# Optimization experiments

Hardware: AMD Instinct MI355X
Metric: run time of the kernel (lower is better)

## Reference

```python
import jax, jax.numpy as jnp
import numpy as np

C = 512
C8 = C // 8
B, H, W = 4, 64, 64


def _conv1x1(x, w, b):
    # x: (B, Cin, H, W), w: (Cout, Cin), b: (Cout,)
    return jnp.einsum('oi,bihw->bohw', w, x) + b[None, :, None, None]


def setup_inputs() -> dict:
    key = jax.random.key(0)
    ks = jax.random.split(key, 16)
    s = 0.02
    inp = {
        'x': jax.random.normal(ks[0], (B, C, H, W), dtype=jnp.float32),
        'wpq': jax.random.normal(ks[1], (C8, C), dtype=jnp.float32) * s,
        'bpq': jnp.zeros((C8,), jnp.float32),
        'wpk': jax.random.normal(ks[2], (C8, C), dtype=jnp.float32) * s,
        'bpk': jnp.zeros((C8,), jnp.float32),
        'wpv': jax.random.normal(ks[3], (C, C), dtype=jnp.float32) * s,
        'bpv': jnp.zeros((C,), jnp.float32),
        'wcq': jax.random.normal(ks[4], (C, C), dtype=jnp.float32) * s,
        'bcq': jnp.zeros((C,), jnp.float32),
        'wck': jax.random.normal(ks[5], (C, C), dtype=jnp.float32) * s,
        'bck': jnp.zeros((C,), jnp.float32),
        'wcv': jax.random.normal(ks[6], (C, C), dtype=jnp.float32) * s,
        'bcv': jnp.zeros((C,), jnp.float32),
        # gammas are zero-init in torch; use small nonzero values so both
        # attention branches contribute to the output numerically.
        'gpos': jax.random.normal(ks[7], (1,), dtype=jnp.float32) * 0.1,
        'gchan': jax.random.normal(ks[8], (1,), dtype=jnp.float32) * 0.1,
    }
    return inp


def reference(x, wpq, bpq, wpk, bpk, wpv, bpv, wcq, bcq, wck, bck, wcv, bcv, gpos, gchan):
    b, c, h, w = x.shape
    n = h * w
    # ---- position attention ----
    pos_q = _conv1x1(x, wpq, bpq).reshape(b, C8, n)           # (b, C/8, N)
    pos_k = _conv1x1(x, wpk, bpk).reshape(b, C8, n)           # (b, C/8, N)
    pos_v = _conv1x1(x, wpv, bpv).reshape(b, c, n)            # (b, C, N)
    pos_attn = jax.nn.softmax(jnp.einsum('bcq,bck->bqk', pos_q, pos_k), axis=-1)  # (b, N, N)
    pos_out = jnp.einsum('bck,bqk->bcq', pos_v, pos_attn).reshape(b, c, h, w)
    pos_out = gpos * pos_out + x
    # ---- channel attention ----
    chan_q = _conv1x1(pos_out, wcq, bcq).reshape(b, c, n)
    chan_k = _conv1x1(pos_out, wck, bck).reshape(b, c, n)
    chan_v = _conv1x1(pos_out, wcv, bcv).reshape(b, c, n)
    chan_attn = jax.nn.softmax(jnp.einsum('bin,bjn->bij', chan_q, chan_k), axis=-1)  # (b, C, C)
    chan_out = jnp.einsum('bij,bjn->bin', chan_attn, chan_v).reshape(b, c, h, w)
    return gchan * chan_out + pos_out
```

## Files before the change

kernel.cpp:

```cpp
#include <hip/hip_runtime.h>
#include <hip/hip_bf16.h>
#include <math.h>

typedef __bf16 bf16;
typedef __attribute__((ext_vector_type(8))) __bf16 bf16x8;
typedef __attribute__((ext_vector_type(4))) __bf16 bf16x4;
typedef __attribute__((ext_vector_type(4))) float f32x4;

#define DEVI static __device__ __forceinline__

DEVI int swzb(int row, int ch) { return ((ch ^ (row & 7)) << 4); }

DEVI void gl_lds16(const void* g, void* l) {
  __builtin_amdgcn_global_load_lds(
      (const __attribute__((address_space(1))) unsigned int*)g,
      (__attribute__((address_space(3))) unsigned int*)l, 16, 0, 0);
}

template<int N> DEVI void wait_vm() {
  if constexpr (N == 0) asm volatile("s_waitcnt vmcnt(0)" ::: "memory");
  else if constexpr (N == 4) asm volatile("s_waitcnt vmcnt(4)" ::: "memory");
  else if constexpr (N == 6) asm volatile("s_waitcnt vmcnt(6)" ::: "memory");
  else if constexpr (N == 8) asm volatile("s_waitcnt vmcnt(8)" ::: "memory");
}
DEVI void sbar() {
  __builtin_amdgcn_sched_barrier(0);
  __builtin_amdgcn_s_barrier();
  __builtin_amdgcn_sched_barrier(0);
}

__global__ __launch_bounds__(256) void prep_weights(
    const float* __restrict__ wpq, const float* __restrict__ wpk,
    const float* __restrict__ wpv, const float* __restrict__ wcq,
    const float* __restrict__ wck, const float* __restrict__ wcv,
    const float* __restrict__ bpq, const float* __restrict__ bpk,
    bf16* __restrict__ wqk, bf16* __restrict__ wpvb, bf16* __restrict__ wcqb,
    bf16* __restrict__ wckb, bf16* __restrict__ wcvT, float* __restrict__ bqk)
{
  int i = blockIdx.x * 256 + threadIdx.x;
  switch (blockIdx.y) {
    case 0: if (i < 64*512)  wqk[i]          = (bf16)wpq[i]; break;
    case 1: if (i < 64*512)  wqk[64*512 + i] = (bf16)wpk[i]; break;
    case 2: if (i < 512*512) wpvb[i] = (bf16)wpv[i]; break;
    case 3: if (i < 512*512) wcqb[i] = (bf16)wcq[i]; break;
    case 4: if (i < 512*512) wckb[i] = (bf16)wck[i]; break;
    case 5: if (i < 512*512) { int t = i >> 9, j = i & 511; wcvT[i] = (bf16)wcv[j*512 + t]; } break;
    case 6: if (i < 64) bqk[i] = bpq[i]; else if (i < 128) bqk[i] = bpk[i - 64]; break;
  }
}

__global__ __launch_bounds__(256) void transpose_x(const float* __restrict__ x, bf16* __restrict__ xbT)
{
  __shared__ float t[32][33];
  int b = blockIdx.z, n0 = blockIdx.x * 32, c0 = blockIdx.y * 32;
  int tx = threadIdx.x & 31, ty = threadIdx.x >> 5;
#pragma unroll
  for (int i = 0; i < 4; ++i)
    t[ty + 8*i][tx] = x[((size_t)b*512 + c0 + ty + 8*i)*4096 + n0 + tx];
  __syncthreads();
#pragma unroll
  for (int i = 0; i < 4; ++i)
    xbT[((size_t)b*4096 + n0 + ty + 8*i)*512 + c0 + tx] = (bf16)t[tx][ty + 8*i];
}

struct GemmP {
  const bf16* A; const bf16* Bt; void* C;
  long aS, bS;
  long cSbytes;
  int lda, ldb, ldc, K;
  int remap;
  const float* biasM; const float* biasN;
  const float* e_bq; const float* e_v; const float* e_u; const float* e_bk; float e_nn;
  long vS, uS;
  const float* gchan; const float* Abv; const bf16* Pres; long abvS, presS;
};

template<int BM, int BN, int BIAS, int EPI>
__global__ __launch_bounds__(256) void gemm_k(GemmP p)
{
  constexpr int QF = BM / 32;
  constexpr int CF = BN / 32;
  constexpr int NBUF = (BM + BN <= 192) ? 3 : 2;
  constexpr int LOADS = (BM + BN) / 32;
  __shared__ __align__(16) char sa[NBUF][BM * 128];
  __shared__ __align__(16) char sb[NBUF][BN * 128];
  const int tid = threadIdx.x, lane = tid & 63, w = tid >> 6;
  const int g = lane >> 4, l15 = lane & 15;
  int bx = blockIdx.x, by = blockIdx.y, bz = blockIdx.z;
  if (p.remap) {
    int ph = blockIdx.x;
    bz = (ph & 7) >> 1;
    int idx = ((ph & 1) << 6) | (ph >> 3);
    bx = idx & 3; by = idx >> 2;
  }
  const int bm = bx * BM, bn = by * BN;
  const bf16* A  = p.A  + (size_t)bz * p.aS;
  const bf16* Bt = p.Bt + (size_t)bz * p.bS;
  char* Cb = (char*)p.C + (size_t)bz * p.cSbytes;
  const int wm = (w & 1) * (BM / 2), wn = (w >> 1) * (BN / 2);
  const int srow = tid >> 3, sch = tid & 7;

  f32x4 acc[QF][CF];
#pragma unroll
  for (int i = 0; i < QF; ++i)
#pragma unroll
    for (int j = 0; j < CF; ++j) acc[i][j] = f32x4{0.f, 0.f, 0.f, 0.f};

  auto stage = [&](int k0, int bi) {
#pragma unroll
    for (int it = 0; it < BM / 32; ++it) {
      int r = it * 32 + srow;
      gl_lds16(A + (size_t)(bm + r) * p.lda + k0 + ((sch ^ (r & 7)) * 8),
               sa[bi] + (it * 32 + w * 8) * 128);
    }
#pragma unroll
    for (int it = 0; it < BN / 32; ++it) {
      int r = it * 32 + srow;
      gl_lds16(Bt + (size_t)(bn + r) * p.ldb + k0 + ((sch ^ (r & 7)) * 8),
               sb[bi] + (it * 32 + w * 8) * 128);
    }
  };
  auto compute = [&](int bi) {
#pragma unroll
    for (int kc = 0; kc < 2; ++kc) {
      bf16x8 af[QF], bfr[CF];
#pragma unroll
      for (int qf = 0; qf < QF; ++qf) {
        int row = wm + 16 * qf + l15;
        af[qf] = *(const bf16x8*)(sa[bi] + row * 128 + swzb(row, g + 4 * kc));
      }
#pragma unroll
      for (int cf = 0; cf < CF; ++cf) {
        int row = wn + 16 * cf + l15;
        bfr[cf] = *(const bf16x8*)(sb[bi] + row * 128 + swzb(row, g + 4 * kc));
      }
      __builtin_amdgcn_s_setprio(1);
#pragma unroll
      for (int qf = 0; qf < QF; ++qf)
#pragma unroll
        for (int cf = 0; cf < CF; ++cf)
          acc[qf][cf] = __builtin_amdgcn_mfma_f32_16x16x32_bf16(af[qf], bfr[cf], acc[qf][cf], 0, 0, 0);
      __builtin_amdgcn_s_setprio(0);
    }
  };

  const int nk = p.K >> 6;
  if constexpr (NBUF == 3) {
    stage(0, 0);
    if (nk > 1) { stage(64, 1); wait_vm<LOADS>(); } else wait_vm<0>();
    sbar();
    int bi = 0;
    for (int t = 0; t < nk; ++t) {
      int b2 = bi + 2; if (b2 >= 3) b2 -= 3;
      if (t + 2 < nk) stage((t + 2) << 6, b2);
      compute(bi);
      if (t + 1 < nk) {
        if (t + 2 < nk) wait_vm<LOADS>(); else wait_vm<0>();
        sbar();
      }
      if (++bi == 3) bi = 0;
    }
  } else {
    stage(0, 0);
    __syncthreads();
    for (int t = 0; t < nk; ++t) {
      const int cur = t & 1;
      if (t + 1 < nk) stage((t + 1) << 6, cur ^ 1);
      compute(cur);
      __syncthreads();
    }
  }

  float gc = 0.f;
  const float* AbvB = nullptr; const bf16* PresB = nullptr;
  const float* eV = nullptr; const float* eU = nullptr;
  if (EPI == 3) { gc = p.gchan[0]; AbvB = p.Abv + (size_t)bz * p.abvS; PresB = p.Pres + (size_t)bz * p.presS; }
  if (EPI == 2) { eV = p.e_v + (size_t)bz * p.vS; eU = p.e_u + (size_t)bz * p.uS; }

#pragma unroll
  for (int qf = 0; qf < QF; ++qf)
#pragma unroll
    for (int cf = 0; cf < CF; ++cf)
#pragma unroll
      for (int r = 0; r < 4; ++r) {
        int m = bm + wm + 16 * qf + 4 * g + r;
        int n = bn + wn + 16 * cf + l15;
        float v = acc[qf][cf][r];
        if (BIAS == 1) v += p.biasM[m];
        if (BIAS == 2) v += p.biasN[n];
        size_t idx = (size_t)m * p.ldc + n;
        if (EPI == 0) ((bf16*)Cb)[idx] = (bf16)v;
        else if (EPI == 1) ((float*)Cb)[idx] = v;
        else if (EPI == 2) {
          v += p.e_bq[m] * eV[n] + eU[m] * p.e_bk[n] + p.e_nn * p.e_bq[m] * p.e_bk[n];
          ((float*)Cb)[idx] = v;
        } else {
          v = gc * (v + AbvB[m]) + (float)PresB[idx];
          ((float*)Cb)[idx] = v;
        }
      }
}

__global__ __launch_bounds__(512, 4) void flash_pos(
    const bf16* __restrict__ QKT, const bf16* __restrict__ Vv,
    const float* __restrict__ x, const float* __restrict__ gpos,
    bf16* __restrict__ Pb, bf16* __restrict__ PTb)
{
  extern __shared__ char sm[];
  char* Vlds = sm + 16384;
  char* Plds = sm + 49152;
  float* Och  = (float*)sm;
  float* lsum = (float*)(sm + 57344);

  const int tid = threadIdx.x, lane = tid & 63, w = tid >> 6;
  const int g = lane >> 4, l15 = lane & 15;
  const int wq = w & 3;
  const int wh = w >> 2;
  const int phys = blockIdx.x;
  const int b  = (phys & 7) >> 1;
  const int ch = phys & 1;
  const int q0 = (phys >> 3) << 6;
  const int c0 = ch << 8;

  const bf16* QKTb = QKT + (size_t)b * 4096 * 128;
  const bf16* Vb   = Vv  + (size_t)b * 512 * 4096;

  const bf16* qrow = QKTb + (size_t)(q0 + 16 * wq + l15) * 128;
  bf16x8 qa0 = *(const bf16x8*)(qrow + 8 * g);
  bf16x8 qa1 = *(const bf16x8*)(qrow + 32 + 8 * g);

  f32x4 acc[4][2];
#pragma unroll
  for (int i = 0; i < 4; ++i) { acc[i][0] = f32x4{0.f,0.f,0.f,0.f}; acc[i][1] = f32x4{0.f,0.f,0.f,0.f}; }
  f32x4 l_r = f32x4{0.f, 0.f, 0.f, 0.f};

  const int srow = tid >> 3, sch = tid & 7;
  const bf16* Ksrc = QKTb + (size_t)srow * 128 + 64 + ((sch ^ (srow & 7)) * 8);

  gl_lds16(Ksrc, sm + w * 1024);
#pragma unroll
  for (int it = 0; it < 4; ++it) {
    int r = it * 64 + srow;
    gl_lds16(Vb + (size_t)(c0 + r) * 4096 + ((sch ^ (r & 7)) * 8),
             Vlds + (it * 64 + w * 8) * 128);
  }
  asm volatile("s_waitcnt vmcnt(0)" ::: "memory");
  sbar();

  for (int t = 0; t < 64; ++t) {
    const char* Kcur = sm + ((t & 1) << 13);
    char* Knext = sm + (((t + 1) & 1) << 13);
    const int ktn = (t + 1) & 63;
    gl_lds16(Ksrc + (size_t)ktn * 8192, Knext + w * 1024);
    __builtin_amdgcn_sched_barrier(0);
    f32x4 s0 = f32x4{0.f,0.f,0.f,0.f}, s1 = f32x4{0.f,0.f,0.f,0.f};
    {
      const int r0 = 32 * wh + l15, r1 = r0 + 16;
      bf16x8 k00 = *(const bf16x8*)(Kcur + r0 * 128 + swzb(r0, g));
      bf16x8 k01 = *(const bf16x8*)(Kcur + r0 * 128 + swzb(r0, g + 4));
      bf16x8 k10 = *(const bf16x8*)(Kcur + r1 * 128 + swzb(r1, g));
      bf16x8 k11 = *(const bf16x8*)(Kcur + r1 * 128 + swzb(r1, g + 4));
      __builtin_amdgcn_s_setprio(1);
      s0 = __builtin_amdgcn_mfma_f32_16x16x32_bf16(qa0, k00, s0, 0, 0, 0);
      s0 = __builtin_amdgcn_mfma_f32_16x16x32_bf16(qa1, k01, s0, 0, 0, 0);
      s1 = __builtin_amdgcn_mfma_f32_16x16x32_bf16(qa0, k10, s1, 0, 0, 0);
      s1 = __builtin_amdgcn_mfma_f32_16x16x32_bf16(qa1, k11, s1, 0, 0, 0);
      __builtin_amdgcn_s_setprio(0);
    }
#pragma unroll
    for (int r = 0; r < 4; ++r) {
      float e0 = __expf(s0[r]), e1 = __expf(s1[r]);
      l_r[r] += e0 + e1;
      int row = 16 * wq + 4 * g + r;
      int ca = 32 * wh + l15, cb = ca + 16;
      *(bf16*)(Plds + row * 128 + (((ca >> 3) ^ (row & 7)) << 4) + ((ca & 7) * 2)) = (bf16)e0;
      *(bf16*)(Plds + row * 128 + (((cb >> 3) ^ (row & 7)) << 4) + ((cb & 7) * 2)) = (bf16)e1;
    }
    asm volatile("s_waitcnt vmcnt(1) lgkmcnt(0)" ::: "memory");
    sbar();
    __builtin_amdgcn_s_setprio(1);
#pragma unroll
    for (int kc = 0; kc < 2; ++kc) {
      const int vra = 32 * w + l15, vrb = vra + 16;
      bf16x8 v0 = *(const bf16x8*)(Vlds + vra * 128 + swzb(vra, g + 4 * kc));
      bf16x8 v1 = *(const bf16x8*)(Vlds + vrb * 128 + swzb(vrb, g + 4 * kc));
#pragma unroll
      for (int qf = 0; qf < 4; ++qf) {
        int row = 16 * qf + l15;
        bf16x8 ap = *(const bf16x8*)(Plds + row * 128 + swzb(row, g + 4 * kc));
        acc[qf][0] = __builtin_amdgcn_mfma_f32_16x16x32_bf16(ap, v0, acc[qf][0], 0, 0, 0);
        acc[qf][1] = __builtin_amdgcn_mfma_f32_16x16x32_bf16(ap, v1, acc[qf][1], 0, 0, 0);
      }
    }
    __builtin_amdgcn_s_setprio(0);
    asm volatile("s_waitcnt vmcnt(0) lgkmcnt(0)" ::: "memory");
    sbar();
#pragma unroll
    for (int it = 0; it < 4; ++it) {
      int r = it * 64 + srow;
      gl_lds16(Vb + (size_t)(c0 + r) * 4096 + ktn * 64 + ((sch ^ (r & 7)) * 8),
               Vlds + (it * 64 + w * 8) * 128);
    }
  }
  asm volatile("s_waitcnt vmcnt(0) lgkmcnt(0)" ::: "memory");
  sbar();

#pragma unroll
  for (int off = 1; off < 16; off <<= 1) {
#pragma unroll
    for (int r = 0; r < 4; ++r) l_r[r] += __shfl_xor(l_r[r], off);
  }
  if (l15 == 0)
#pragma unroll
    for (int r = 0; r < 4; ++r) lsum[wh * 64 + 16 * wq + 4 * g + r] = l_r[r];
  __syncthreads();

  const float gp = gpos[0];
  for (int j = 0; j < 2; ++j) {
    if ((w >> 2) == j) {
#pragma unroll
      for (int qf = 0; qf < 4; ++qf) {
        float inv[4];
#pragma unroll
        for (int r = 0; r < 4; ++r) {
          int qi = 16 * qf + 4 * g + r;
          inv[r] = gp / (lsum[qi] + lsum[64 + qi]);
        }
#pragma unroll
        for (int cf = 0; cf < 2; ++cf) {
          int cl = 32 * (w & 3) + 16 * cf + l15;
#pragma unroll
          for (int r = 0; r < 4; ++r)
            Och[cl * 68 + 16 * qf + 4 * g + r] = acc[qf][cf][r] * inv[r];
        }
      }
    }
    __syncthreads();
    {
      int cl = tid >> 2, qs = (tid & 3) * 16;
      int cg = c0 + 128 * j + cl;
      const float* xr = x + ((size_t)b * 512 + cg) * 4096 + q0 + qs;
      float* och = Och + cl * 68 + qs;
      float tmp[16];
#pragma unroll
      for (int i = 0; i < 16; ++i) { tmp[i] = och[i] + xr[i]; och[i] = tmp[i]; }
      bf16x8 o0, o1;
#pragma unroll
      for (int i = 0; i < 8; ++i) { o0[i] = (bf16)tmp[i]; o1[i] = (bf16)tmp[i + 8]; }
      bf16* pr = Pb + ((size_t)b * 512 + cg) * 4096 + q0 + qs;
      *(bf16x8*)pr = o0; *(bf16x8*)(pr + 8) = o1;
    }
    __syncthreads();
    {
      int q = tid >> 3, cs = (tid & 7) * 16;
      float tmp[16];
#pragma unroll
      for (int i = 0; i < 16; ++i) tmp[i] = Och[(cs + i) * 68 + q];
      bf16x8 o0, o1;
#pragma unroll
      for (int i = 0; i < 8; ++i) { o0[i] = (bf16)tmp[i]; o1[i] = (bf16)tmp[i + 8]; }
      bf16* pt = PTb + ((size_t)b * 4096 + q0 + q) * 512 + c0 + 128 * j + cs;
      *(bf16x8*)pt = o0; *(bf16x8*)(pt + 8) = o1;
    }
    __syncthreads();
  }
}

__global__ __launch_bounds__(256) void row_sum(const bf16* __restrict__ Pb, float* __restrict__ r)
{
  int wid = blockIdx.x * 4 + (threadIdx.x >> 6);
  int lane = threadIdx.x & 63;
  const bf16* row = Pb + (size_t)wid * 4096;
  float s = 0.f;
#pragma unroll
  for (int i = 0; i < 8; ++i) {
    bf16x8 v = ((const bf16x8*)row)[lane + 64 * i];
#pragma unroll
    for (int j = 0; j < 8; ++j) s += (float)v[j];
  }
#pragma unroll
  for (int off = 1; off < 64; off <<= 1) s += __shfl_xor(s, off);
  if (lane == 0) r[wid] = s;
}

__global__ __launch_bounds__(256) void uv_kernel(
    const float* __restrict__ wcq, const float* __restrict__ wck,
    const float* __restrict__ r, float* __restrict__ u, float* __restrict__ v)
{
  int b = blockIdx.z;
  int i = blockIdx.x * 256 + threadIdx.x;
  const float* rb = r + b * 512;
  const float* wrow = (blockIdx.y ? wck : wcq) + (size_t)i * 512;
  float s = 0.f;
  for (int t = 0; t < 512; ++t) s += wrow[t] * rb[t];
  (blockIdx.y ? v : u)[b * 512 + i] = s;
}

__global__ __launch_bounds__(256) void softmax_chan(
    const float* __restrict__ L, const float* __restrict__ bcv,
    bf16* __restrict__ Ab, float* __restrict__ Abv)
{
  int b = blockIdx.z;
  int i = blockIdx.x * 4 + (threadIdx.x >> 6);
  int lane = threadIdx.x & 63;
  const float* row = L + ((size_t)b * 512 + i) * 512;
  f32x4 v0 = ((const f32x4*)row)[lane];
  f32x4 v1 = ((const f32x4*)row)[lane + 64];
  float mx = fmaxf(fmaxf(fmaxf(v0[0], v0[1]), fmaxf(v0[2], v0[3])),
                   fmaxf(fmaxf(v1[0], v1[1]), fmaxf(v1[2], v1[3])));
#pragma unroll
  for (int off = 1; off < 64; off <<= 1) mx = fmaxf(mx, __shfl_xor(mx, off));
  float e[8]; float s = 0.f;
#pragma unroll
  for (int k = 0; k < 4; ++k) { e[k] = __expf(v0[k] - mx); s += e[k]; }
#pragma unroll
  for (int k = 0; k < 4; ++k) { e[4 + k] = __expf(v1[k] - mx); s += e[4 + k]; }
#pragma unroll
  for (int off = 1; off < 64; off <<= 1) s += __shfl_xor(s, off);
  float inv = 1.f / s;
  bf16x4 a0, a1;
  const f32x4 bv0 = ((const f32x4*)bcv)[lane];
  const f32x4 bv1 = ((const f32x4*)bcv)[lane + 64];
  float pb = 0.f;
#pragma unroll
  for (int k = 0; k < 4; ++k) {
    float p0 = e[k] * inv, p1 = e[4 + k] * inv;
    a0[k] = (bf16)p0; a1[k] = (bf16)p1;
    pb += p0 * bv0[k] + p1 * bv1[k];
  }
  bf16* arow = Ab + ((size_t)b * 512 + i) * 512;
  *(bf16x4*)(arow + 4 * lane) = a0;
  *(bf16x4*)(arow + 256 + 4 * lane) = a1;
#pragma unroll
  for (int off = 1; off < 64; off <<= 1) pb += __shfl_xor(pb, off);
  if (lane == 0) Abv[b * 512 + i] = pb;
}

extern "C" void kernel_launch(void* const* d_in, const int* in_sizes, int n_in,
                              void* d_out, int out_size, void* d_ws, size_t ws_size,
                              hipStream_t stream)
{
  const float* x    = (const float*)d_in[0];
  const float* wpq  = (const float*)d_in[1];
  const float* bpq  = (const float*)d_in[2];
  const float* wpk  = (const float*)d_in[3];
  const float* bpk  = (const float*)d_in[4];
  const float* wpv  = (const float*)d_in[5];
  const float* bpv  = (const float*)d_in[6];
  const float* wcq  = (const float*)d_in[7];
  const float* bcq  = (const float*)d_in[8];
  const float* wck  = (const float*)d_in[9];
  const float* bck  = (const float*)d_in[10];
  const float* wcv  = (const float*)d_in[11];
  const float* bcv  = (const float*)d_in[12];
  const float* gpos = (const float*)d_in[13];
  const float* gch  = (const float*)d_in[14];
  float* out = (float*)d_out;

  char* ws = (char*)d_ws;
  size_t off = 0;
  auto alloc = [&](size_t bytes) -> char* {
    char* p = ws + off; off = (off + bytes + 255) & ~(size_t)255; return p;
  };
  bf16*  xbT  = (bf16*)alloc(4UL * 4096 * 512 * 2);
  bf16*  QKT  = (bf16*)alloc(4UL * 4096 * 128 * 2);
  bf16*  V    = (bf16*)alloc(4UL * 512 * 4096 * 2);
  bf16*  Pb   = (bf16*)alloc(4UL * 512 * 4096 * 2);
  bf16*  PTb  = (bf16*)alloc(4UL * 4096 * 512 * 2);
  bf16*  G    = (bf16*)alloc(4UL * 512 * 512 * 2);
  bf16*  M1   = (bf16*)alloc(4UL * 512 * 512 * 2);
  float* Lws  = (float*)alloc(4UL * 512 * 512 * 4);
  bf16*  Ab   = (bf16*)alloc(4UL * 512 * 512 * 2);
  bf16*  B2   = (bf16*)alloc(4UL * 512 * 512 * 2);
  bf16*  wqk  = (bf16*)alloc(128UL * 512 * 2);
  bf16*  wpvb = (bf16*)alloc(512UL * 512 * 2);
  bf16*  wcqb = (bf16*)alloc(512UL * 512 * 2);
  bf16*  wckb = (bf16*)alloc(512UL * 512 * 2);
  bf16*  wcvT = (bf16*)alloc(512UL * 512 * 2);
  float* bqk  = (float*)alloc(128 * 4);
  float* rws  = (float*)alloc(4UL * 512 * 4);
  float* uws  = (float*)alloc(4UL * 512 * 4);
  float* vws  = (float*)alloc(4UL * 512 * 4);
  float* Abv  = (float*)alloc(4UL * 512 * 4);
  if (off > ws_size) return;

  prep_weights<<<dim3(1024, 7, 1), 256, 0, stream>>>(wpq, wpk, wpv, wcq, wck, wcv,
                                                     bpq, bpk, wqk, wpvb, wcqb, wckb, wcvT, bqk);
  transpose_x<<<dim3(128, 16, 4), 256, 0, stream>>>(x, xbT);

  GemmP p{};
  p = GemmP{};
  p.A = xbT; p.aS = 4096L * 512; p.lda = 512;
  p.Bt = wqk; p.bS = 0; p.ldb = 512;
  p.C = QKT; p.cSbytes = 4096L * 128 * 2; p.ldc = 128;
  p.K = 512; p.biasN = bqk;
  gemm_k<128, 64, 2, 0><<<dim3(32, 2, 4), 256, 0, stream>>>(p);

  p = GemmP{};
  p.A = wpvb; p.aS = 0; p.lda = 512;
  p.Bt = xbT; p.bS = 4096L * 512; p.ldb = 512;
  p.C = V; p.cSbytes = 512L * 4096 * 2; p.ldc = 4096;
  p.K = 512; p.biasM = bpv; p.remap = 1;
  gemm_k<128, 128, 1, 0><<<dim3(512, 1, 1), 256, 0, stream>>>(p);

  flash_pos<<<dim3(512, 1, 1), 512, 57856, stream>>>(QKT, V, x, gpos, Pb, PTb);

  p = GemmP{};
  p.A = Pb; p.aS = 512L * 4096; p.lda = 4096;
  p.Bt = Pb; p.bS = 512L * 4096; p.ldb = 4096;
  p.C = G; p.cSbytes = 512L * 512 * 2; p.ldc = 512;
  p.K = 4096;
  gemm_k<64, 64, 0, 0><<<dim3(8, 8, 4), 256, 0, stream>>>(p);

  row_sum<<<dim3(512, 1, 1), 256, 0, stream>>>(Pb, rws);
  uv_kernel<<<dim3(2, 2, 4), 256, 0, stream>>>(wcq, wck, rws, uws, vws);

  p = GemmP{};
  p.A = wcqb; p.aS = 0; p.lda = 512;
  p.Bt = G; p.bS = 512L * 512; p.ldb = 512;
  p.C = M1; p.cSbytes = 512L * 512 * 2; p.ldc = 512;
  p.K = 512;
  gemm_k<64, 64, 0, 0><<<dim3(8, 8, 4), 256, 0, stream>>>(p);

  p = GemmP{};
  p.A = M1; p.aS = 512L * 512; p.lda = 512;
  p.Bt = wckb; p.bS = 0; p.ldb = 512;
  p.C = Lws; p.cSbytes = 512L * 512 * 4; p.ldc = 512;
  p.K = 512;
  p.e_bq = bcq; p.e_v = vws; p.vS = 512; p.e_u = uws; p.uS = 512; p.e_bk = bck; p.e_nn = 4096.f;
  gemm_k<64, 64, 0, 2><<<dim3(8, 8, 4), 256, 0, stream>>>(p);

  softmax_chan<<<dim3(128, 1, 4), 256, 0, stream>>>(Lws, bcv, Ab, Abv);

  p = GemmP{};
  p.A = Ab; p.aS = 512L * 512; p.lda = 512;
  p.Bt = wcvT; p.bS = 0; p.ldb = 512;
  p.C = B2; p.cSbytes = 512L * 512 * 2; p.ldc = 512;
  p.K = 512;
  gemm_k<64, 64, 0, 0><<<dim3(8, 8, 4), 256, 0, stream>>>(p);

  p = GemmP{};
  p.A = B2; p.aS = 512L * 512; p.lda = 512;
  p.Bt = PTb; p.bS = 4096L * 512; p.ldb = 512;
  p.C = out; p.cSbytes = 512L * 4096 * 4; p.ldc = 4096;
  p.K = 512;
  p.gchan = gch; p.Abv = Abv; p.abvS = 512; p.Pres = Pb; p.presS = 512L * 4096;
  p.remap = 1;
  gemm_k<128, 128, 0, 3><<<dim3(512, 1, 1), 256, 0, stream>>>(p);
}
```

Measured before the change: 267.3 us.

## Exploit Gram symmetry with triangular tiling and shrink the large GEMM tiles

The Gram GEMM G = P·Pᵀ (K=4096) now launches only the lower-triangular 64x64 tiles (36 per batch instead of 64). Each tile also writes its transpose, using the symmetry of G to cut its MMA work roughly in half. The V projection and final output GEMMs move from 128x128 to 128x64 tiles with twice as many blocks, and the remap is generalised to use gridDim. uv_kernel is vectorised to float4 loads. The transposed stores in the triangular kernel are strided and uncoalesced, and smaller tiles reduce operand reuse.

```diff
diff --git a/kernel.cpp b/kernel.cpp
--- a/kernel.cpp
+++ b/kernel.cpp
@@ -75,7 +75,7 @@
   const float* gchan; const float* Abv; const bf16* Pres; long abvS, presS;
 };
 
-template<int BM, int BN, int BIAS, int EPI>
+template<int BM, int BN, int BIAS, int EPI, bool TRI>
 __global__ __launch_bounds__(256) void gemm_k(GemmP p)
 {
   constexpr int QF = BM / 32;
@@ -87,10 +87,15 @@
   const int tid = threadIdx.x, lane = tid & 63, w = tid >> 6;
   const int g = lane >> 4, l15 = lane & 15;
   int bx = blockIdx.x, by = blockIdx.y, bz = blockIdx.z;
-  if (p.remap) {
+  if (TRI) {
+    int rem = blockIdx.x, i = 0;
+    while (rem >= i + 1) { rem -= i + 1; ++i; }
+    bx = i; by = rem;
+  } else if (p.remap) {
     int ph = blockIdx.x;
+    int per = (int)(gridDim.x >> 3);
     bz = (ph & 7) >> 1;
-    int idx = ((ph & 1) << 6) | (ph >> 3);
+    int idx = (ph & 1) * per + (ph >> 3);
     bx = idx & 3; by = idx >> 2;
   }
   const int bm = bx * BM, bn = by * BN;
@@ -189,7 +194,10 @@
         if (BIAS == 1) v += p.biasM[m];
         if (BIAS == 2) v += p.biasN[n];
         size_t idx = (size_t)m * p.ldc + n;
-        if (EPI == 0) ((bf16*)Cb)[idx] = (bf16)v;
+        if (EPI == 0) {
+          ((bf16*)Cb)[idx] = (bf16)v;
+          if (TRI) ((bf16*)Cb)[(size_t)n * p.ldc + m] = (bf16)v;
+        }
         else if (EPI == 1) ((float*)Cb)[idx] = v;
         else if (EPI == 2) {
           v += p.e_bq[m] * eV[n] + eU[m] * p.e_bk[n] + p.e_nn * p.e_bq[m] * p.e_bk[n];
@@ -389,10 +397,13 @@
 {
   int b = blockIdx.z;
   int i = blockIdx.x * 256 + threadIdx.x;
-  const float* rb = r + b * 512;
-  const float* wrow = (blockIdx.y ? wck : wcq) + (size_t)i * 512;
+  const f32x4* rb = (const f32x4*)(r + b * 512);
+  const f32x4* wrow = (const f32x4*)((blockIdx.y ? wck : wcq) + (size_t)i * 512);
   float s = 0.f;
-  for (int t = 0; t < 512; ++t) s += wrow[t] * rb[t];
+  for (int t = 0; t < 128; ++t) {
+    f32x4 a = wrow[t], c = rb[t];
+    s += a[0]*c[0] + a[1]*c[1] + a[2]*c[2] + a[3]*c[3];
+  }
   (blockIdx.y ? v : u)[b * 512 + i] = s;
 }
 
@@ -494,14 +505,14 @@
   p.Bt = wqk; p.bS = 0; p.ldb = 512;
   p.C = QKT; p.cSbytes = 4096L * 128 * 2; p.ldc = 128;
   p.K = 512; p.biasN = bqk;
-  gemm_k<128, 64, 2, 0><<<dim3(32, 2, 4), 256, 0, stream>>>(p);
+  gemm_k<128, 64, 2, 0, false><<<dim3(32, 2, 4), 256, 0, stream>>>(p);
 
   p = GemmP{};
   p.A = wpvb; p.aS = 0; p.lda = 512;
   p.Bt = xbT; p.bS = 4096L * 512; p.ldb = 512;
   p.C = V; p.cSbytes = 512L * 4096 * 2; p.ldc = 4096;
   p.K = 512; p.biasM = bpv; p.remap = 1;
-  gemm_k<128, 128, 1, 0><<<dim3(512, 1, 1), 256, 0, stream>>>(p);
+  gemm_k<128, 64, 1, 0, false><<<dim3(1024, 1, 1), 256, 0, stream>>>(p);
 
   flash_pos<<<dim3(512, 1, 1), 512, 57856, stream>>>(QKT, V, x, gpos, Pb, PTb);
 
@@ -510,7 +521,7 @@
   p.Bt = Pb; p.bS = 512L * 4096; p.ldb = 4096;
   p.C = G; p.cSbytes = 512L * 512 * 2; p.ldc = 512;
   p.K = 4096;
-  gemm_k<64, 64, 0, 0><<<dim3(8, 8, 4), 256, 0, stream>>>(p);
+  gemm_k<64, 64, 0, 0, true><<<dim3(36, 1, 4), 256, 0, stream>>>(p);
 
   row_sum<<<dim3(512, 1, 1), 256, 0, stream>>>(Pb, rws);
   uv_kernel<<<dim3(2, 2, 4), 256, 0, stream>>>(wcq, wck, rws, uws, vws);
@@ -520,7 +531,7 @@
   p.Bt = G; p.bS = 512L * 512; p.ldb = 512;
   p.C = M1; p.cSbytes = 512L * 512 * 2; p.ldc = 512;
   p.K = 512;
-  gemm_k<64, 64, 0, 0><<<dim3(8, 8, 4), 256, 0, stream>>>(p);
+  gemm_k<64, 64, 0, 0, false><<<dim3(8, 8, 4), 256, 0, stream>>>(p);
 
   p = GemmP{};
   p.A = M1; p.aS = 512L * 512; p.lda = 512;
@@ -528,7 +539,7 @@
   p.C = Lws; p.cSbytes = 512L * 512 * 4; p.ldc = 512;
   p.K = 512;
   p.e_bq = bcq; p.e_v = vws; p.vS = 512; p.e_u = uws; p.uS = 512; p.e_bk = bck; p.e_nn = 4096.f;
-  gemm_k<64, 64, 0, 2><<<dim3(8, 8, 4), 256, 0, stream>>>(p);
+  gemm_k<64, 64, 0, 2, false><<<dim3(8, 8, 4), 256, 0, stream>>>(p);
 
   softmax_chan<<<dim3(128, 1, 4), 256, 0, stream>>>(Lws, bcv, Ab, Abv);
 
@@ -537,7 +548,7 @@
   p.Bt = wcvT; p.bS = 0; p.ldb = 512;
   p.C = B2; p.cSbytes = 512L * 512 * 2; p.ldc = 512;
   p.K = 512;
-  gemm_k<64, 64, 0, 0><<<dim3(8, 8, 4), 256, 0, stream>>>(p);
+  gemm_k<64, 64, 0, 0, false><<<dim3(8, 8, 4), 256, 0, stream>>>(p);
 
   p = GemmP{};
   p.A = B2; p.aS = 512L * 512; p.lda = 512;
@@ -546,5 +557,5 @@
   p.K = 512;
   p.gchan = gch; p.Abv = Abv; p.abvS = 512; p.Pres = Pb; p.presS = 512L * 4096;
   p.remap = 1;
-  gemm_k<128, 128, 0, 3><<<dim3(512, 1, 1), 256, 0, stream>>>(p);
-}
+  gemm_k<128, 64, 0, 3, false><<<dim3(1024, 1, 1), 256, 0, stream>>>(p);
+}
```

Result: slower. 275.7 us (+3.1%).
